# Kernel tuning notes

Measured on AMD Instinct MI355X. Metric: run time of the kernel, lower is better.

Reference implementation:

```python
import jax, jax.numpy as jnp
import numpy as np

H = 64       # hidden size hard-coded in the module
NH = 4       # n_heads
S = 500      # stock_num
D = 10       # num_day
T = 40       # num_text (news per day)
FP = 3       # price features
FT = 512     # text embedding dim


def gru_scan(x, Wih, Whh, bih, bhh):
    """Single-sequence GRU (torch gate convention). x: (T, F) -> hidden states (T, H)."""
    gi = x @ Wih + bih  # (T, 3H) precompute input gates outside the scan

    def step(h, g):
        gh = h @ Whh + bhh
        r = jax.nn.sigmoid(g[:H] + gh[:H])
        z = jax.nn.sigmoid(g[H:2 * H] + gh[H:2 * H])
        n = jnp.tanh(g[2 * H:] + r * gh[2 * H:])
        h_new = (1.0 - z) * n + z * h
        return h_new, h_new

    h0 = jnp.zeros((H,), x.dtype)
    _, hs = jax.lax.scan(step, h0, gi)
    return hs


def attn_pool(hs, W, v):
    """Additive attention pooling over time. hs: (T, H) -> (H,)."""
    scores = jnp.tanh(hs @ W) @ v          # (T,)
    alpha = jax.nn.softmax(scores)
    return alpha @ hs


def _gru_params(key, fin, scale=0.08):
    k1, k2, k3, k4 = jax.random.split(key, 4)
    return (jax.random.normal(k1, (S, fin, 3 * H)) * scale,
            jax.random.normal(k2, (S, H, 3 * H)) * scale,
            jax.random.normal(k3, (S, 3 * H)) * scale,
            jax.random.normal(k4, (S, 3 * H)) * scale)


def _attn_params(key, scale=0.08):
    k1, k2 = jax.random.split(key)
    return (jax.random.normal(k1, (S, H, H)) * scale,
            jax.random.normal(k2, (S, H)) * scale)


def setup_inputs() -> dict:
    key = jax.random.key(0)
    ks = jax.random.split(key, 20)
    inp = {}
    inp['text_input'] = jax.random.normal(ks[0], (S, D, T, FT), dtype=jnp.float32)
    inp['price_input'] = jax.random.normal(ks[1], (S, D, FP), dtype=jnp.float32)
    inp['label'] = jax.random.randint(ks[2], (S,), 0, 2)
    inp['adj'] = jnp.ones((S, S), dtype=jnp.float32)
    inp['train'] = 0
    # per-stock stacked parameters
    (inp['Wih_p'], inp['Whh_p'], inp['bih_p'], inp['bhh_p']) = _gru_params(ks[3], FP)
    (inp['Wa_p'], inp['va_p']) = _attn_params(ks[4])
    (inp['Wih_t'], inp['Whh_t'], inp['bih_t'], inp['bhh_t']) = _gru_params(ks[5], FT)
    (inp['Wa_t'], inp['va_t']) = _attn_params(ks[6])
    (inp['Wih_s'], inp['Whh_s'], inp['bih_s'], inp['bhh_s']) = _gru_params(ks[7], H)
    (inp['Wa_s'], inp['va_s']) = _attn_params(ks[8])
    inp['Wb'] = jax.random.normal(ks[9], (S, H, H, H)) * 0.05   # Bilinear weight (out,in1,in2)
    inp['bb'] = jax.random.normal(ks[10], (S, H)) * 0.05
    inp['Wbl'] = jax.random.normal(ks[11], (S, H, 2)) * 0.08
    inp['bbl'] = jax.random.normal(ks[12], (S, 2)) * 0.08
    # shared cross-stock self-attention projections and final fc
    inp['Wq'] = jax.random.normal(ks[13], (H, H)) * 0.08
    inp['bq'] = jax.random.normal(ks[14], (H,)) * 0.08
    inp['Wk'] = jax.random.normal(ks[15], (H, H)) * 0.08
    inp['bk'] = jax.random.normal(ks[16], (H,)) * 0.08
    inp['Wf'] = jax.random.normal(ks[17], (H, 2)) * 0.08
    inp['bf'] = jax.random.normal(ks[18], (2,)) * 0.08
    return inp


def _forward(text_input, price_input, label,
             Wih_p, Whh_p, bih_p, bhh_p, Wa_p, va_p,
             Wih_t, Whh_t, bih_t, bhh_t, Wa_t, va_t,
             Wih_s, Whh_s, bih_s, bhh_s, Wa_s, va_s,
             Wb, bb, Wbl, bbl, Wq, bq, Wk, bk, Wf, bf):
    # ---- per-stock price encoder: GRU over days + attention pooling ----
    def enc_price(x, a, b, c, d, W, v):
        return attn_pool(gru_scan(x, a, b, c, d), W, v)
    x_price = jax.vmap(enc_price)(price_input, Wih_p, Whh_p, bih_p, bhh_p, Wa_p, va_p)  # (S, H)

    # ---- per-stock, per-day text encoder ----
    def enc_text_stock(xdays, a, b, c, d, W, v):
        return jax.vmap(lambda x: attn_pool(gru_scan(x, a, b, c, d), W, v))(xdays)  # (D, H)
    news = jax.vmap(enc_text_stock)(text_input, Wih_t, Whh_t, bih_t, bhh_t, Wa_t, va_t)  # (S, D, H)

    # ---- per-stock sequence encoder over days ----
    text_vec = jax.vmap(enc_price)(news, Wih_s, Whh_s, bih_s, bhh_s, Wa_s, va_s)  # (S, H)

    # ---- bilinear fusion: tanh(Bilinear(text, price)) ----
    combined = jnp.tanh(jnp.einsum('si,skij,sj->sk', text_vec, Wb, x_price) + bb)  # (S, H)

    # ---- per-stock blending head ----
    out_1 = jnp.tanh(jnp.einsum('si,sik->sk', combined, Wbl) + bbl)  # (S, 2)

    # ---- cross-stock multi-head self-attention (q,k projected, v identity) ----
    dh = H // NH
    q = (combined @ Wq + bq).reshape(S, NH, dh)
    k = (combined @ Wk + bk).reshape(S, NH, dh)
    v = combined.reshape(S, NH, dh)
    scores = jnp.einsum('shd,thd->hst', q, k) / (dh ** 0.5)
    attn = jax.nn.softmax(scores, axis=-1)
    attn_out = jnp.einsum('hst,thd->shd', attn, v).reshape(S, H)

    x = jax.nn.elu(attn_out @ Wf + bf)  # (S, 2)
    output = jax.nn.softmax(x + out_1, axis=1)
    # faithful to the original: CrossEntropyLoss applied to already-softmaxed output
    logp = jax.nn.log_softmax(output, axis=1)
    loss = -jnp.mean(logp[jnp.arange(S), label])
    return loss, output


def reference(text_input, price_input, label, adj, train,
              Wih_p, Whh_p, bih_p, bhh_p, Wa_p, va_p,
              Wih_t, Whh_t, bih_t, bhh_t, Wa_t, va_t,
              Wih_s, Whh_s, bih_s, bhh_s, Wa_s, va_s,
              Wb, bb, Wbl, bbl, Wq, bq, Wk, bk, Wf, bf):
    return _forward(text_input, price_input, label,
                    Wih_p, Whh_p, bih_p, bhh_p, Wa_p, va_p,
                    Wih_t, Whh_t, bih_t, bhh_t, Wa_t, va_t,
                    Wih_s, Whh_s, bih_s, bhh_s, Wa_s, va_s,
                    Wb, bb, Wbl, bbl, Wq, bq, Wk, bk, Wf, bf)
```

## Files before the change

kernel.cpp:

```cpp
#include <hip/hip_runtime.h>

#define Sn 500
#define Dn 10
#define Tn 40
#define FPn 3
#define FTn 512
#define Hn 64
#define G3 192
#define NHn 4

typedef __attribute__((ext_vector_type(8))) short bf8_t;
typedef __attribute__((ext_vector_type(4))) float f4_t;

__device__ __forceinline__ unsigned short f2bf(float f) {
    union { float f; unsigned int u; } v; v.f = f;
    unsigned int r = v.u + 0x7fffu + ((v.u >> 16) & 1u);
    return (unsigned short)(r >> 16);
}
__device__ __forceinline__ float bflo(unsigned int u) {
    union { unsigned int u; float f; } v; v.u = u << 16; return v.f;
}
__device__ __forceinline__ float bfhi(unsigned int u) {
    union { unsigned int u; float f; } v; v.u = u & 0xffff0000u; return v.f;
}
__device__ __forceinline__ unsigned int cvtpk(float lo, float hi) {
    unsigned int r;
    asm("v_cvt_pk_bf16_f32 %0, %1, %2" : "=v"(r) : "v"(lo), "v"(hi));
    return r;
}
__device__ __forceinline__ float sigmoidf_(float x) { return 1.f / (1.f + __expf(-x)); }
__device__ __forceinline__ float tanhf_(float x) {
    x = fminf(15.f, fmaxf(-15.f, x));
    float e = __expf(2.f * x);
    return (e - 1.f) / (e + 1.f);
}
__device__ __forceinline__ float dot8(uint4 wv, f4_t hA, f4_t hB) {
    return bflo(wv.x) * hA[0] + bfhi(wv.x) * hA[1]
         + bflo(wv.y) * hA[2] + bfhi(wv.y) * hA[3]
         + bflo(wv.z) * hB[0] + bfhi(wv.z) * hB[1]
         + bflo(wv.w) * hB[2] + bfhi(wv.w) * hB[3];
}
union bfu { bf8_t v; unsigned int u[4]; };

__global__ __launch_bounds__(64, 1) void price_gru(
    const float* __restrict__ price, const float* __restrict__ Wih_p,
    const float* __restrict__ Whh_p, const float* __restrict__ bih_p,
    const float* __restrict__ bhh_p, const float* __restrict__ Wa_p,
    const float* __restrict__ va_p, float* __restrict__ xprice)
{
    __shared__ __align__(16) unsigned char smp[33160];
    unsigned char* whh2 = smp;
    unsigned char* wa2 = smp + 24576;
    float* hbuf = (float*)(smp + 32768);
    float* priceL = (float*)(smp + 33040);

    const int s = blockIdx.x, l = threadIdx.x;
    {
        const float* W3 = Whh_p + (size_t)s * Hn * G3;
        for (int r = 0; r < 192; ++r) {
            int e = l + r * 64, i = e / G3, j = e - i * G3;
            *(unsigned short*)(whh2 + j * 128 + ((2 * i) ^ ((j & 7) << 4))) = f2bf(W3[e]);
        }
        const float* A3 = Wa_p + (size_t)s * Hn * Hn;
        for (int r = 0; r < 64; ++r) {
            int e = l + r * 64, i = e >> 6, k = e & 63;
            *(unsigned short*)(wa2 + k * 128 + ((2 * i) ^ ((k & 7) << 4))) = f2bf(A3[e]);
        }
        if (l < 30) priceL[l] = price[(size_t)s * 30 + l];
        hbuf[l] = 0.f;
        if (l < 4) hbuf[64 + l] = 0.f;
    }
    __builtin_amdgcn_wave_barrier();
    {
        float wp[3][3];
        #pragma unroll
        for (int i = 0; i < 3; ++i)
            #pragma unroll
            for (int g = 0; g < 3; ++g)
                wp[i][g] = Wih_p[(size_t)s * 3 * G3 + i * G3 + g * 64 + l];
        const float bi0 = bih_p[(size_t)s * G3 + l];
        const float bi1 = bih_p[(size_t)s * G3 + 64 + l];
        const float bi2 = bih_p[(size_t)s * G3 + 128 + l];
        const float bh0 = bhh_p[(size_t)s * G3 + l];
        const float bh1 = bhh_p[(size_t)s * G3 + 64 + l];
        const float bh2 = bhh_p[(size_t)s * G3 + 128 + l];
        const float vak = va_p[(size_t)s * Hn + l];
        const int swl = (l & 7) << 4;
        float h3 = 0.f, m3 = -1e30f, den3 = 0.f, av3 = 0.f;
        for (int t = 0; t < Dn; ++t) {
            float x0 = priceL[t * 3], x1 = priceL[t * 3 + 1], x2 = priceL[t * 3 + 2];
            float gg0 = bi0 + x0 * wp[0][0] + x1 * wp[1][0] + x2 * wp[2][0];
            float gg1 = bi1 + x0 * wp[0][1] + x1 * wp[1][1] + x2 * wp[2][1];
            float gg2 = bi2 + x0 * wp[0][2] + x1 * wp[1][2] + x2 * wp[2][2];
            float gh0 = bh0, gh1 = bh1, gh2 = bh2;
            #pragma unroll
            for (int ic = 0; ic < 8; ++ic) {
                const int off = (ic * 16) ^ swl;
                f4_t hA = *(const f4_t*)&hbuf[ic * 8];
                f4_t hB = *(const f4_t*)&hbuf[ic * 8 + 4];
                uint4 w0 = *(const uint4*)(whh2 + l * 128 + off);
                uint4 w1 = *(const uint4*)(whh2 + (l + 64) * 128 + off);
                uint4 w2 = *(const uint4*)(whh2 + (l + 128) * 128 + off);
                gh0 += dot8(w0, hA, hB); gh1 += dot8(w1, hA, hB); gh2 += dot8(w2, hA, hB);
            }
            float r = sigmoidf_(gg0 + gh0);
            float z = sigmoidf_(gg1 + gh1);
            float n = tanhf_(gg2 + r * gh2);
            h3 = (1.f - z) * n + z * h3;
            __builtin_amdgcn_wave_barrier();
            hbuf[l] = h3;
            __builtin_amdgcn_wave_barrier();
            float sk = 0.f;
            #pragma unroll
            for (int ic = 0; ic < 8; ++ic) {
                const int off = (ic * 16) ^ swl;
                uint4 wv = *(const uint4*)(wa2 + l * 128 + off);
                f4_t hA = *(const f4_t*)&hbuf[ic * 8];
                f4_t hB = *(const f4_t*)&hbuf[ic * 8 + 4];
                sk += dot8(wv, hA, hB);
            }
            float term = tanhf_(sk) * vak;
            #pragma unroll
            for (int off = 32; off; off >>= 1) term += __shfl_xor(term, off);
            float mn = fmaxf(m3, term);
            float s0 = __expf(m3 - mn);
            float p = __expf(term - mn);
            den3 = den3 * s0 + p;
            av3 = av3 * s0 + p * h3;
            m3 = mn;
        }
        xprice[(size_t)s * Hn + l] = av3 / den3;
    }
}

__global__ __launch_bounds__(256) void k1_mega(
    const float* __restrict__ text, const float* __restrict__ Wih,
    const float* __restrict__ bih, float* __restrict__ gi2,
    const float* __restrict__ Wb, const float* __restrict__ xprice,
    float* __restrict__ u)
{
    __shared__ __align__(16) unsigned char sm[18688];

    const int bid = blockIdx.x, tid = threadIdx.x;
    const int xcd = bid & 7, ix = bid >> 3;
    const int swz = (xcd < 4 ? xcd * 563 : 2252 + (xcd - 4) * 562) + ix;
    const int grp = swz / 9, sub = swz - grp * 9;
    const int w = tid >> 6, l = tid & 63;

    if (sub < 5) {
        const int s = grp, fi = sub;
        const int lr = l & 15, kg = l >> 4;
        unsigned short* Asb = (unsigned short*)sm;
        unsigned char*  Bsb = sm + 6400;

        const float* xbase = text + ((size_t)s * 400 + fi * 80) * FTn;
        const float* Wihs  = Wih + (size_t)s * FTn * G3;

        f4_t acc[5][3];
        #pragma unroll
        for (int a = 0; a < 5; a++)
            #pragma unroll
            for (int b = 0; b < 3; b++) acc[a][b] = (f4_t){0.f, 0.f, 0.f, 0.f};

        f4_t pa[3];
        f4_t pb0[3], pb1[3];

        auto aload = [&](int kk) {
            #pragma unroll
            for (int q = 0; q < 3; ++q) {
                int t = tid + q * 256;
                if (q < 2 || tid < 128) {
                    int row = t >> 3, ch = t & 7;
                    pa[q] = *(const f4_t*)(xbase + (size_t)row * FTn + kk * 32 + ch * 4);
                }
            }
        };
        auto bload = [&](int kk) {
            #pragma unroll
            for (int q = 0; q < 3; ++q) {
                int t = tid + q * 256;
                int kp = t / 48, cq = t % 48;
                const float* p = Wihs + (size_t)(kk * 32 + 2 * kp) * G3 + cq * 4;
                pb0[q] = *(const f4_t*)p;
                pb1[q] = *(const f4_t*)(p + G3);
            }
        };
        auto awrite = [&]() {
            #pragma unroll
            for (int q = 0; q < 3; ++q) {
                int t = tid + q * 256;
                if (q < 2 || tid < 128) {
                    int row = t >> 3, ch = t & 7;
                    uint2 uu = { cvtpk(pa[q][0], pa[q][1]), cvtpk(pa[q][2], pa[q][3]) };
                    *(uint2*)((unsigned char*)Asb + row * 80 + ch * 8) = uu;
                }
            }
        };
        auto bwrite = [&]() {
            #pragma unroll
            for (int q = 0; q < 3; ++q) {
                int t = tid + q * 256;
                int kp = t / 48, cq = t % 48;
                int base = (kp >> 2) * 3072 + (kp & 3) * 4;
                #pragma unroll
                for (int i = 0; i < 4; ++i) {
                    int col = cq * 4 + i;
                    int colp = col ^ ((col >> 2) & 7);
                    *(unsigned int*)(Bsb + base + colp * 16) = cvtpk(pb0[q][i], pb1[q][i]);
                }
            }
        };

        aload(0); bload(0);
        for (int kk = 0; kk < 16; ++kk) {
            awrite(); bwrite();
            __syncthreads();
            if (kk < 15) { aload(kk + 1); bload(kk + 1); }
            bf8_t bfr[3];
            #pragma unroll
            for (int nc = 0; nc < 3; ++nc) {
                int col = w * 48 + nc * 16 + lr;
                int colp = col ^ ((col >> 2) & 7);
                bfr[nc] = *(const bf8_t*)(Bsb + kg * 3072 + colp * 16);
            }
            #pragma unroll
            for (int mt = 0; mt < 5; ++mt) {
                bf8_t af = *(const bf8_t*)((unsigned char*)Asb + (mt * 16 + lr) * 80 + kg * 16);
                acc[mt][0] = __builtin_amdgcn_mfma_f32_16x16x32_bf16(af, bfr[0], acc[mt][0], 0, 0, 0);
                acc[mt][1] = __builtin_amdgcn_mfma_f32_16x16x32_bf16(af, bfr[1], acc[mt][1], 0, 0, 0);
                acc[mt][2] = __builtin_amdgcn_mfma_f32_16x16x32_bf16(af, bfr[2], acc[mt][2], 0, 0, 0);
            }
            __syncthreads();
        }

        const float* bihs = bih + (size_t)s * G3 + w * 48 + lr;
        #pragma unroll
        for (int nc = 0; nc < 3; ++nc) {
            const int col = w * 48 + nc * 16 + lr;
            const float bv = bihs[nc * 16];
            #pragma unroll
            for (int mt = 0; mt < 5; ++mt)
                #pragma unroll
                for (int rg = 0; rg < 4; ++rg) {
                    int r = mt * 16 + kg * 4 + rg;
                    int hi = (r >= 40);
                    int day = fi * 2 + hi;
                    int t = r - hi * 40;
                    gi2[((size_t)(s * 40 + t) * 10 + day) * 192 + col] = acc[mt][nc][rg] + bv;
                }
        }
    } else {
        const int s = grp, kq = sub - 5;
        float* uT = (float*)sm;
        const int j4 = (l & 15) * 4;
        f4_t xq = *(const f4_t*)&xprice[s * Hn + j4];

        const float* Wbs = Wb + (size_t)s * Hn * Hn * Hn;
        for (int g = 0; g < 64; ++g) {
            int P = kq * 1024 + w * 256 + g * 4 + (l >> 4);
            f4_t wv = *(const f4_t*)&Wbs[(size_t)P * Hn + j4];
            float dp = wv[0] * xq[0] + wv[1] * xq[1] + wv[2] * xq[2] + wv[3] * xq[3];
            dp += __shfl_xor(dp, 8);
            dp += __shfl_xor(dp, 4);
            dp += __shfl_xor(dp, 2);
            dp += __shfl_xor(dp, 1);
            if ((l & 15) == 0) { int k = P >> 6, i = P & 63; uT[i * 17 + (k - kq * 16)] = dp; }
        }
        __syncthreads();
        #pragma unroll
        for (int r = 0; r < 4; ++r) {
            int flat = tid + r * 256;
            int kr = flat >> 6, i = flat & 63;
            u[((size_t)s * 64 + kq * 16 + kr) * 64 + i] = uT[i * 17 + kr];
        }
    }
}

__global__ __launch_bounds__(64, 1) void gru_text_f(
    const float* __restrict__ gi2, const float* __restrict__ Whh,
    const float* __restrict__ bhh, const float* __restrict__ Wa,
    const float* __restrict__ va, float* __restrict__ news)
{
    __shared__ __align__(16) float hrow[16 * 68];
    __shared__ __align__(16) unsigned char waT[Hn * 128];

    const int s = blockIdx.x, l = threadIdx.x;
    const int lr = l & 15, lg = l >> 4;

    const float* Whhs = Whh + (size_t)s * Hn * G3;
    bfu bwhh[2][12];
    #pragma unroll
    for (int ks = 0; ks < 2; ++ks)
        #pragma unroll
        for (int nt = 0; nt < 12; ++nt) {
            const float* p = Whhs + (size_t)(ks * 32 + lg * 8) * G3 + nt * 16 + lr;
            float b0 = p[0], b1 = p[G3], b2 = p[2 * G3], b3 = p[3 * G3];
            float b4 = p[4 * G3], b5 = p[5 * G3], b6 = p[6 * G3], b7 = p[7 * G3];
            bwhh[ks][nt].u[0] = cvtpk(b0, b1); bwhh[ks][nt].u[1] = cvtpk(b2, b3);
            bwhh[ks][nt].u[2] = cvtpk(b4, b5); bwhh[ks][nt].u[3] = cvtpk(b6, b7);
        }
    float bhh_l[12];
    #pragma unroll
    for (int nt = 0; nt < 12; ++nt) bhh_l[nt] = bhh[(size_t)s * G3 + nt * 16 + lr];
    float va_l[4];
    #pragma unroll
    for (int nt = 0; nt < 4; ++nt) va_l[nt] = va[(size_t)s * Hn + nt * 16 + lr];

    {
        const float* Was = Wa + (size_t)s * Hn * Hn;
        for (int r = 0; r < 64; ++r) {
            int e = l + r * 64, i = e >> 6, k = e & 63;
            *(unsigned short*)(waT + k * 128 + ((2 * i) ^ ((k & 7) << 4))) = f2bf(Was[e]);
        }
        #pragma unroll
        for (int r = 0; r < 17; ++r) hrow[l + r * 64] = 0.f;
    }
    __builtin_amdgcn_wave_barrier();

    int dayoff[4];
    #pragma unroll
    for (int rr = 0; rr < 4; ++rr) {
        int d = lg * 4 + rr; if (d > 9) d = 9;
        dayoff[rr] = d * 192 + lr;
    }
    const float* gbase = gi2 + (size_t)s * 40 * 1920;

    float val[48], valn[48];
    #pragma unroll
    for (int j = 0; j < 48; ++j) val[j] = gbase[dayoff[j & 3] + (j >> 2) * 16];

    bf8_t a0f, a1f;
    {   bfu z0; z0.u[0] = 0; z0.u[1] = 0; z0.u[2] = 0; z0.u[3] = 0; a0f = z0.v; a1f = z0.v; }

    float h[4][4], accv[4][4], den[4], m[4];
    #pragma unroll
    for (int nt = 0; nt < 4; ++nt)
        #pragma unroll
        for (int rr = 0; rr < 4; ++rr) { h[nt][rr] = 0.f; accv[nt][rr] = 0.f; }
    #pragma unroll
    for (int rr = 0; rr < 4; ++rr) { den[rr] = 0.f; m[rr] = -1e30f; }

    for (int t = 0; t < Tn; ++t) {
        f4_t acc[12];
        #pragma unroll
        for (int nt = 0; nt < 12; ++nt)
            acc[nt] = (f4_t){bhh_l[nt], bhh_l[nt], bhh_l[nt], bhh_l[nt]};
        __builtin_amdgcn_s_setprio(1);
        #pragma unroll
        for (int nt = 0; nt < 12; ++nt) {
            acc[nt] = __builtin_amdgcn_mfma_f32_16x16x32_bf16(a0f, bwhh[0][nt].v, acc[nt], 0, 0, 0);
            acc[nt] = __builtin_amdgcn_mfma_f32_16x16x32_bf16(a1f, bwhh[1][nt].v, acc[nt], 0, 0, 0);
        }
        __builtin_amdgcn_s_setprio(0);
        {
            const int tn = (t < Tn - 1) ? t + 1 : t;
            const float* gb = gbase + (size_t)tn * 1920;
            #pragma unroll
            for (int j = 0; j < 48; ++j) valn[j] = gb[dayoff[j & 3] + (j >> 2) * 16];
        }
        #pragma unroll
        for (int nt = 0; nt < 4; ++nt)
            #pragma unroll
            for (int rr = 0; rr < 4; ++rr) {
                float r = sigmoidf_(val[nt * 4 + rr] + acc[nt][rr]);
                float z = sigmoidf_(val[(nt + 4) * 4 + rr] + acc[nt + 4][rr]);
                float n = tanhf_(val[(nt + 8) * 4 + rr] + r * acc[nt + 8][rr]);
                h[nt][rr] = (1.f - z) * n + z * h[nt][rr];
            }
        __builtin_amdgcn_wave_barrier();
        #pragma unroll
        for (int rr = 0; rr < 4; ++rr) {
            int day = lg * 4 + rr;
            if (day < Dn) {
                #pragma unroll
                for (int nt = 0; nt < 4; ++nt) hrow[day * 68 + nt * 16 + lr] = h[nt][rr];
            }
        }
        __builtin_amdgcn_wave_barrier();
        {
            const float* hp = hrow + lr * 68 + lg * 8;
            f4_t x0 = *(const f4_t*)hp,        x1 = *(const f4_t*)(hp + 4);
            f4_t y0 = *(const f4_t*)(hp + 32), y1 = *(const f4_t*)(hp + 36);
            bfu t0, t1;
            t0.u[0] = cvtpk(x0[0], x0[1]); t0.u[1] = cvtpk(x0[2], x0[3]);
            t0.u[2] = cvtpk(x1[0], x1[1]); t0.u[3] = cvtpk(x1[2], x1[3]);
            t1.u[0] = cvtpk(y0[0], y0[1]); t1.u[1] = cvtpk(y0[2], y0[3]);
            t1.u[2] = cvtpk(y1[0], y1[1]); t1.u[3] = cvtpk(y1[2], y1[3]);
            a0f = t0.v; a1f = t1.v;
        }
        f4_t sc[4];
        #pragma unroll
        for (int nt = 0; nt < 4; ++nt) sc[nt] = (f4_t){0.f, 0.f, 0.f, 0.f};
        __builtin_amdgcn_s_setprio(1);
        #pragma unroll
        for (int ks = 0; ks < 2; ++ks) {
            bf8_t av = ks ? a1f : a0f;
            #pragma unroll
            for (int nt = 0; nt < 4; ++nt) {
                bf8_t bwv = *(const bf8_t*)(waT + (nt * 16 + lr) * 128
                                            + ((ks * 64 + lg * 16) ^ ((lr & 7) << 4)));
                sc[nt] = __builtin_amdgcn_mfma_f32_16x16x32_bf16(av, bwv, sc[nt], 0, 0, 0);
            }
        }
        __builtin_amdgcn_s_setprio(0);
        float pr[4];
        #pragma unroll
        for (int rr = 0; rr < 4; ++rr) {
            pr[rr] = tanhf_(sc[0][rr]) * va_l[0] + tanhf_(sc[1][rr]) * va_l[1]
                   + tanhf_(sc[2][rr]) * va_l[2] + tanhf_(sc[3][rr]) * va_l[3];
            pr[rr] += __shfl_xor(pr[rr], 1);
            pr[rr] += __shfl_xor(pr[rr], 2);
            pr[rr] += __shfl_xor(pr[rr], 4);
            pr[rr] += __shfl_xor(pr[rr], 8);
        }
        #pragma unroll
        for (int rr = 0; rr < 4; ++rr) {
            float mn = fmaxf(m[rr], pr[rr]);
            float s0 = __expf(m[rr] - mn);
            float p = __expf(pr[rr] - mn);
            den[rr] = den[rr] * s0 + p;
            #pragma unroll
            for (int nt = 0; nt < 4; ++nt)
                accv[nt][rr] = accv[nt][rr] * s0 + p * h[nt][rr];
            m[rr] = mn;
        }
        #pragma unroll
        for (int j = 0; j < 48; ++j) val[j] = valn[j];
    }
    #pragma unroll
    for (int rr = 0; rr < 4; ++rr) {
        int day = lg * 4 + rr;
        if (day < Dn) {
            float inv = 1.f / den[rr];
            #pragma unroll
            for (int nt = 0; nt < 4; ++nt)
                news[((size_t)s * Dn + day) * Hn + nt * 16 + lr] = accv[nt][rr] * inv;
        }
    }
}

__global__ __launch_bounds__(64, 1) void day_finish(
    const float* __restrict__ news,
    const float* __restrict__ Wih_s, const float* __restrict__ Whh_s,
    const float* __restrict__ bih_s, const float* __restrict__ bhh_s,
    const float* __restrict__ Wa_s, const float* __restrict__ va_s,
    const float* __restrict__ u, const float* __restrict__ bb,
    const float* __restrict__ Wq, const float* __restrict__ bq,
    const float* __restrict__ Wk, const float* __restrict__ bk,
    const float* __restrict__ Wbl, const float* __restrict__ bbl,
    float* __restrict__ combined, float* __restrict__ qg,
    float* __restrict__ kg, float* __restrict__ out1)
{
    __shared__ __align__(16) unsigned char sm[60928];
    unsigned char* whh2 = sm;
    unsigned char* wih2 = sm + 24576;
    unsigned char* wa2 = sm + 49152;
    float* newsL = (float*)(sm + 57600);
    float* hbuf  = (float*)(sm + 60320);

    const int s = blockIdx.x, l = threadIdx.x;
    float tvv;

    {
        const float* W2 = Whh_s + (size_t)s * Hn * G3;
        const float* X2 = Wih_s + (size_t)s * Hn * G3;
        for (int r = 0; r < 192; ++r) {
            int e = l + r * 64, i = e / G3, j = e - i * G3;
            int off = j * 128 + ((2 * i) ^ ((j & 7) << 4));
            *(unsigned short*)(whh2 + off) = f2bf(W2[e]);
            *(unsigned short*)(wih2 + off) = f2bf(X2[e]);
        }
        const float* A2 = Wa_s + (size_t)s * Hn * Hn;
        for (int r = 0; r < 64; ++r) {
            int e = l + r * 64, i = e >> 6, k = e & 63;
            *(unsigned short*)(wa2 + k * 128 + ((2 * i) ^ ((k & 7) << 4))) = f2bf(A2[e]);
        }
        #pragma unroll
        for (int d = 0; d < Dn; ++d) newsL[d * 68 + l] = news[((size_t)s * Dn + d) * Hn + l];
        hbuf[l] = 0.f;
        if (l < 4) hbuf[64 + l] = 0.f;
    }
    __builtin_amdgcn_wave_barrier();
    {
        const float bi0 = bih_s[(size_t)s * G3 + l];
        const float bi1 = bih_s[(size_t)s * G3 + 64 + l];
        const float bi2 = bih_s[(size_t)s * G3 + 128 + l];
        const float bh0 = bhh_s[(size_t)s * G3 + l];
        const float bh1 = bhh_s[(size_t)s * G3 + 64 + l];
        const float bh2 = bhh_s[(size_t)s * G3 + 128 + l];
        const float vak = va_s[(size_t)s * Hn + l];
        const int swl = (l & 7) << 4;
        float h2 = 0.f, m2 = -1e30f, den2 = 0.f, av2 = 0.f;
        for (int t = 0; t < Dn; ++t) {
            float gh0 = bh0, gh1 = bh1, gh2 = bh2;
            float gg0 = bi0, gg1 = bi1, gg2 = bi2;
            #pragma unroll
            for (int ic = 0; ic < 8; ++ic) {
                const int off = (ic * 16) ^ swl;
                f4_t hA = *(const f4_t*)&hbuf[ic * 8];
                f4_t hB = *(const f4_t*)&hbuf[ic * 8 + 4];
                f4_t nA = *(const f4_t*)&newsL[t * 68 + ic * 8];
                f4_t nB = *(const f4_t*)&newsL[t * 68 + ic * 8 + 4];
                uint4 w0 = *(const uint4*)(whh2 + l * 128 + off);
                uint4 w1 = *(const uint4*)(whh2 + (l + 64) * 128 + off);
                uint4 w2 = *(const uint4*)(whh2 + (l + 128) * 128 + off);
                uint4 x0 = *(const uint4*)(wih2 + l * 128 + off);
                uint4 x1 = *(const uint4*)(wih2 + (l + 64) * 128 + off);
                uint4 x2 = *(const uint4*)(wih2 + (l + 128) * 128 + off);
                gh0 += dot8(w0, hA, hB); gh1 += dot8(w1, hA, hB); gh2 += dot8(w2, hA, hB);
                gg0 += dot8(x0, nA, nB); gg1 += dot8(x1, nA, nB); gg2 += dot8(x2, nA, nB);
            }
            float r = sigmoidf_(gg0 + gh0);
            float z = sigmoidf_(gg1 + gh1);
            float n = tanhf_(gg2 + r * gh2);
            h2 = (1.f - z) * n + z * h2;
            __builtin_amdgcn_wave_barrier();
            hbuf[l] = h2;
            __builtin_amdgcn_wave_barrier();
            float sk = 0.f;
            #pragma unroll
            for (int ic = 0; ic < 8; ++ic) {
                const int off = (ic * 16) ^ swl;
                uint4 wv = *(const uint4*)(wa2 + l * 128 + off);
                f4_t hA = *(const f4_t*)&hbuf[ic * 8];
                f4_t hB = *(const f4_t*)&hbuf[ic * 8 + 4];
                sk += dot8(wv, hA, hB);
            }
            float term = tanhf_(sk) * vak;
            #pragma unroll
            for (int off = 32; off; off >>= 1) term += __shfl_xor(term, off);
            float mn = fmaxf(m2, term);
            float s0 = __expf(m2 - mn);
            float p = __expf(term - mn);
            den2 = den2 * s0 + p;
            av2 = av2 * s0 + p * h2;
            m2 = mn;
        }
        tvv = av2 / den2;
    }
    __builtin_amdgcn_wave_barrier();

    float* uL = (float*)sm;
    float* tvL = (float*)(sm + 16640);
    float* cl  = (float*)(sm + 16960);
    tvL[l] = tvv;
    const float* ub = u + (size_t)s * 4096;
    #pragma unroll 8
    for (int i = 0; i < 64; ++i) uL[i * 65 + l] = ub[i * 64 + l];
    __builtin_amdgcn_wave_barrier();
    {
        float a = bb[s * Hn + l];
        #pragma unroll 8
        for (int i = 0; i < 64; ++i) a += tvL[i] * uL[l * 65 + i];
        float c = tanhf_(a);
        cl[l] = c;
        combined[s * Hn + l] = c;
    }
    __builtin_amdgcn_wave_barrier();
    {
        float aq = bq[l], ak = bk[l];
        for (int i = 0; i < Hn; i++) {
            float ci = cl[i];
            aq += ci * Wq[i * Hn + l];
            ak += ci * Wk[i * Hn + l];
        }
        qg[s * Hn + l] = aq; kg[s * Hn + l] = ak;
        if (l < 2) {
            float a = bbl[s * 2 + l];
            for (int i = 0; i < Hn; i++) a += cl[i] * Wbl[(size_t)s * Hn * 2 + i * 2 + l];
            out1[s * 2 + l] = tanhf_(a);
        }
    }
}

__global__ __launch_bounds__(256) void mhsa(
    const float* __restrict__ qg, const float* __restrict__ kg,
    const float* __restrict__ combined, const float* __restrict__ Wf,
    const float* __restrict__ bfp, const float* __restrict__ out1,
    float* __restrict__ dout)
{
    __shared__ __align__(16) float ql[Hn];
    __shared__ float sl[NHn][Sn];
    __shared__ float hsum[NHn];
    __shared__ float ao[Hn];
    __shared__ float red2[8];
    __shared__ float red3[4][Hn];

    const int sq = blockIdx.x, tid = threadIdx.x;
    if (tid < Hn) ql[tid] = qg[sq * Hn + tid];
    __syncthreads();

    for (int id = tid; id < Sn * NHn; id += 256) {
        int t = id >> 2, h = id & 3;
        const float* kp = &kg[t * Hn + h * 16];
        float a = 0.f;
        #pragma unroll
        for (int x = 0; x < 16; x += 4) {
            f4_t kv = *(const f4_t*)&kp[x];
            f4_t qv = *(const f4_t*)&ql[h * 16 + x];
            a += kv[0] * qv[0] + kv[1] * qv[1] + kv[2] * qv[2] + kv[3] * qv[3];
        }
        sl[h][t] = a * 0.25f;
    }
    __syncthreads();
    for (int h = 0; h < NHn; ++h) {
        float m = -1e30f;
        for (int t = tid; t < Sn; t += 256) m = fmaxf(m, sl[h][t]);
        for (int o = 32; o; o >>= 1) m = fmaxf(m, __shfl_xor(m, o));
        if ((tid & 63) == 0) red2[tid >> 6] = m;
        __syncthreads();
        m = fmaxf(fmaxf(red2[0], red2[1]), fmaxf(red2[2], red2[3]));
        float ps = 0.f;
        for (int t = tid; t < Sn; t += 256) { float p = __expf(sl[h][t] - m); sl[h][t] = p; ps += p; }
        for (int o = 32; o; o >>= 1) ps += __shfl_xor(ps, o);
        if ((tid & 63) == 0) red2[4 + (tid >> 6)] = ps;
        __syncthreads();
        if (tid == 0) hsum[h] = red2[4] + red2[5] + red2[6] + red2[7];
        __syncthreads();
    }
    {
        const int q = tid >> 6, j = tid & 63, h = j >> 4;
        float a = 0.f;
        for (int t = q * 125; t < q * 125 + 125; ++t) a += sl[h][t] * combined[t * Hn + j];
        red3[q][j] = a;
    }
    __syncthreads();
    if (tid < Hn)
        ao[tid] = (red3[0][tid] + red3[1][tid] + red3[2][tid] + red3[3][tid]) / hsum[tid >> 4];
    __syncthreads();
    if (tid == 0) {
        float l0 = bfp[0], l1 = bfp[1];
        for (int j = 0; j < Hn; j++) { float v = ao[j]; l0 += v * Wf[j * 2]; l1 += v * Wf[j * 2 + 1]; }
        l0 = l0 > 0.f ? l0 : __expf(l0) - 1.f;
        l1 = l1 > 0.f ? l1 : __expf(l1) - 1.f;
        l0 += out1[sq * 2]; l1 += out1[sq * 2 + 1];
        float m = fmaxf(l0, l1);
        float e0 = __expf(l0 - m), e1 = __expf(l1 - m);
        float inv = 1.f / (e0 + e1);
        dout[1 + sq * 2] = e0 * inv;
        dout[2 + sq * 2] = e1 * inv;
    }
}

__global__ __launch_bounds__(512) void loss_k(float* __restrict__ dout,
                                              const int* __restrict__ label)
{
    __shared__ float red[512];
    const int tid = threadIdx.x;
    float a = 0.f;
    if (tid < Sn) {
        float p0 = dout[1 + 2 * tid], p1 = dout[2 + 2 * tid];
        float m = fmaxf(p0, p1);
        float lse = m + __logf(__expf(p0 - m) + __expf(p1 - m));
        float pl = label[tid] ? p1 : p0;
        a = -(pl - lse);
    }
    red[tid] = a;
    __syncthreads();
    for (int o = 256; o; o >>= 1) {
        if (tid < o) red[tid] += red[tid + o];
        __syncthreads();
    }
    if (tid == 0) dout[0] = red[0] / (float)Sn;
}

extern "C" void kernel_launch(void* const* d_in, const int* in_sizes, int n_in,
                              void* d_out, int out_size, void* d_ws, size_t ws_size,
                              hipStream_t stream)
{
    const float* text  = (const float*)d_in[0];
    const float* price = (const float*)d_in[1];
    const int*   label = (const int*)  d_in[2];
    const float* Wih_p = (const float*)d_in[5];
    const float* Whh_p = (const float*)d_in[6];
    const float* bih_p = (const float*)d_in[7];
    const float* bhh_p = (const float*)d_in[8];
    const float* Wa_p  = (const float*)d_in[9];
    const float* va_p  = (const float*)d_in[10];
    const float* Wih_t = (const float*)d_in[11];
    const float* Whh_t = (const float*)d_in[12];
    const float* bih_t = (const float*)d_in[13];
    const float* bhh_t = (const float*)d_in[14];
    const float* Wa_t  = (const float*)d_in[15];
    const float* va_t  = (const float*)d_in[16];
    const float* Wih_s = (const float*)d_in[17];
    const float* Whh_s = (const float*)d_in[18];
    const float* bih_s = (const float*)d_in[19];
    const float* bhh_s = (const float*)d_in[20];
    const float* Wa_s  = (const float*)d_in[21];
    const float* va_s  = (const float*)d_in[22];
    const float* Wb    = (const float*)d_in[23];
    const float* bb    = (const float*)d_in[24];
    const float* Wbl   = (const float*)d_in[25];
    const float* bbl   = (const float*)d_in[26];
    const float* Wq    = (const float*)d_in[27];
    const float* bq    = (const float*)d_in[28];
    const float* Wk    = (const float*)d_in[29];
    const float* bk    = (const float*)d_in[30];
    const float* Wf    = (const float*)d_in[31];
    const float* bf_   = (const float*)d_in[32];

    float* ws = (float*)d_ws;
    float* news     = ws;
    float* xprice   = ws + 320000;
    float* combined = ws + 384000;
    float* qg       = ws + 416000;
    float* kg       = ws + 448000;
    float* out1     = ws + 480000;
    float* u        = ws + 481000;
    float* gi2      = ws + 2529000;
    float* dout = (float*)d_out;

    price_gru<<<Sn, 64, 0, stream>>>(price, Wih_p, Whh_p, bih_p, bhh_p, Wa_p, va_p, xprice);
    k1_mega<<<4500, 256, 0, stream>>>(text, Wih_t, bih_t, gi2, Wb, xprice, u);
    gru_text_f<<<Sn, 64, 0, stream>>>(gi2, Whh_t, bhh_t, Wa_t, va_t, news);
    day_finish<<<Sn, 64, 0, stream>>>(news,
                                      Wih_s, Whh_s, bih_s, bhh_s, Wa_s, va_s,
                                      u, bb, Wq, bq, Wk, bk, Wbl, bbl,
                                      combined, qg, kg, out1);
    mhsa<<<Sn, 256, 0, stream>>>(qg, kg, combined, Wf, bf_, out1, dout);
    loss_k<<<1, 512, 0, stream>>>(dout, label);
}
```

Measured before the change: 580.9 us.

## Double-buffer k1 LDS tiles and fuse text GRU with day-level kernel

The k1_mega GEMM now uses two LDS buffers. The next tile is converted and written while the current one feeds the MFMAs, which removes one barrier per k-step but doubles LDS per block and may lower occupancy. The text-GRU kernel is also merged into the day-level kernel. The per-day news vectors now stay in shared memory instead of going through global memory, and one launch is dropped.

```diff
diff --git a/kernel.cpp b/kernel.cpp
--- a/kernel.cpp
+++ b/kernel.cpp
@@ -139,7 +139,7 @@
     const float* __restrict__ Wb, const float* __restrict__ xprice,
     float* __restrict__ u)
 {
-    __shared__ __align__(16) unsigned char sm[18688];
+    __shared__ __align__(16) unsigned char sm[37376];
 
     const int bid = blockIdx.x, tid = threadIdx.x;
     const int xcd = bid & 7, ix = bid >> 3;
@@ -150,8 +150,8 @@
     if (sub < 5) {
         const int s = grp, fi = sub;
         const int lr = l & 15, kg = l >> 4;
-        unsigned short* Asb = (unsigned short*)sm;
-        unsigned char*  Bsb = sm + 6400;
+        unsigned char* Ab0 = sm;
+        unsigned char* Ab1 = sm + 18688;
 
         const float* xbase = text + ((size_t)s * 400 + fi * 80) * FTn;
         const float* Wihs  = Wih + (size_t)s * FTn * G3;
@@ -185,51 +185,55 @@
                 pb1[q] = *(const f4_t*)(p + G3);
             }
         };
-        auto awrite = [&]() {
+        auto awrite = [&](unsigned char* base) {
             #pragma unroll
             for (int q = 0; q < 3; ++q) {
                 int t = tid + q * 256;
                 if (q < 2 || tid < 128) {
                     int row = t >> 3, ch = t & 7;
                     uint2 uu = { cvtpk(pa[q][0], pa[q][1]), cvtpk(pa[q][2], pa[q][3]) };
-                    *(uint2*)((unsigned char*)Asb + row * 80 + ch * 8) = uu;
+                    *(uint2*)(base + row * 80 + ch * 8) = uu;
                 }
             }
         };
-        auto bwrite = [&]() {
+        auto bwrite = [&](unsigned char* base) {
             #pragma unroll
             for (int q = 0; q < 3; ++q) {
                 int t = tid + q * 256;
                 int kp = t / 48, cq = t % 48;
-                int base = (kp >> 2) * 3072 + (kp & 3) * 4;
+                int off = (kp >> 2) * 3072 + (kp & 3) * 4;
                 #pragma unroll
                 for (int i = 0; i < 4; ++i) {
                     int col = cq * 4 + i;
                     int colp = col ^ ((col >> 2) & 7);
-                    *(unsigned int*)(Bsb + base + colp * 16) = cvtpk(pb0[q][i], pb1[q][i]);
+                    *(unsigned int*)(base + 6400 + off + colp * 16) = cvtpk(pb0[q][i], pb1[q][i]);
                 }
             }
         };
 
         aload(0); bload(0);
+        awrite(Ab0); bwrite(Ab0);
+        __syncthreads();
+
         for (int kk = 0; kk < 16; ++kk) {
-            awrite(); bwrite();
-            __syncthreads();
+            unsigned char* cur = (kk & 1) ? Ab1 : Ab0;
+            unsigned char* nxt = (kk & 1) ? Ab0 : Ab1;
             if (kk < 15) { aload(kk + 1); bload(kk + 1); }
             bf8_t bfr[3];
             #pragma unroll
             for (int nc = 0; nc < 3; ++nc) {
                 int col = w * 48 + nc * 16 + lr;
                 int colp = col ^ ((col >> 2) & 7);
-                bfr[nc] = *(const bf8_t*)(Bsb + kg * 3072 + colp * 16);
+                bfr[nc] = *(const bf8_t*)(cur + 6400 + kg * 3072 + colp * 16);
             }
             #pragma unroll
             for (int mt = 0; mt < 5; ++mt) {
-                bf8_t af = *(const bf8_t*)((unsigned char*)Asb + (mt * 16 + lr) * 80 + kg * 16);
+                bf8_t af = *(const bf8_t*)(cur + (mt * 16 + lr) * 80 + kg * 16);
                 acc[mt][0] = __builtin_amdgcn_mfma_f32_16x16x32_bf16(af, bfr[0], acc[mt][0], 0, 0, 0);
                 acc[mt][1] = __builtin_amdgcn_mfma_f32_16x16x32_bf16(af, bfr[1], acc[mt][1], 0, 0, 0);
                 acc[mt][2] = __builtin_amdgcn_mfma_f32_16x16x32_bf16(af, bfr[2], acc[mt][2], 0, 0, 0);
             }
+            if (kk < 15) { awrite(nxt); bwrite(nxt); }
             __syncthreads();
         }
 
@@ -276,171 +280,10 @@
     }
 }
 
-__global__ __launch_bounds__(64, 1) void gru_text_f(
+__global__ __launch_bounds__(64, 1) void text_day(
     const float* __restrict__ gi2, const float* __restrict__ Whh,
     const float* __restrict__ bhh, const float* __restrict__ Wa,
-    const float* __restrict__ va, float* __restrict__ news)
-{
-    __shared__ __align__(16) float hrow[16 * 68];
-    __shared__ __align__(16) unsigned char waT[Hn * 128];
-
-    const int s = blockIdx.x, l = threadIdx.x;
-    const int lr = l & 15, lg = l >> 4;
-
-    const float* Whhs = Whh + (size_t)s * Hn * G3;
-    bfu bwhh[2][12];
-    #pragma unroll
-    for (int ks = 0; ks < 2; ++ks)
-        #pragma unroll
-        for (int nt = 0; nt < 12; ++nt) {
-            const float* p = Whhs + (size_t)(ks * 32 + lg * 8) * G3 + nt * 16 + lr;
-            float b0 = p[0], b1 = p[G3], b2 = p[2 * G3], b3 = p[3 * G3];
-            float b4 = p[4 * G3], b5 = p[5 * G3], b6 = p[6 * G3], b7 = p[7 * G3];
-            bwhh[ks][nt].u[0] = cvtpk(b0, b1); bwhh[ks][nt].u[1] = cvtpk(b2, b3);
-            bwhh[ks][nt].u[2] = cvtpk(b4, b5); bwhh[ks][nt].u[3] = cvtpk(b6, b7);
-        }
-    float bhh_l[12];
-    #pragma unroll
-    for (int nt = 0; nt < 12; ++nt) bhh_l[nt] = bhh[(size_t)s * G3 + nt * 16 + lr];
-    float va_l[4];
-    #pragma unroll
-    for (int nt = 0; nt < 4; ++nt) va_l[nt] = va[(size_t)s * Hn + nt * 16 + lr];
-
-    {
-        const float* Was = Wa + (size_t)s * Hn * Hn;
-        for (int r = 0; r < 64; ++r) {
-            int e = l + r * 64, i = e >> 6, k = e & 63;
-            *(unsigned short*)(waT + k * 128 + ((2 * i) ^ ((k & 7) << 4))) = f2bf(Was[e]);
-        }
-        #pragma unroll
-        for (int r = 0; r < 17; ++r) hrow[l + r * 64] = 0.f;
-    }
-    __builtin_amdgcn_wave_barrier();
-
-    int dayoff[4];
-    #pragma unroll
-    for (int rr = 0; rr < 4; ++rr) {
-        int d = lg * 4 + rr; if (d > 9) d = 9;
-        dayoff[rr] = d * 192 + lr;
-    }
-    const float* gbase = gi2 + (size_t)s * 40 * 1920;
-
-    float val[48], valn[48];
-    #pragma unroll
-    for (int j = 0; j < 48; ++j) val[j] = gbase[dayoff[j & 3] + (j >> 2) * 16];
-
-    bf8_t a0f, a1f;
-    {   bfu z0; z0.u[0] = 0; z0.u[1] = 0; z0.u[2] = 0; z0.u[3] = 0; a0f = z0.v; a1f = z0.v; }
-
-    float h[4][4], accv[4][4], den[4], m[4];
-    #pragma unroll
-    for (int nt = 0; nt < 4; ++nt)
-        #pragma unroll
-        for (int rr = 0; rr < 4; ++rr) { h[nt][rr] = 0.f; accv[nt][rr] = 0.f; }
-    #pragma unroll
-    for (int rr = 0; rr < 4; ++rr) { den[rr] = 0.f; m[rr] = -1e30f; }
-
-    for (int t = 0; t < Tn; ++t) {
-        f4_t acc[12];
-        #pragma unroll
-        for (int nt = 0; nt < 12; ++nt)
-            acc[nt] = (f4_t){bhh_l[nt], bhh_l[nt], bhh_l[nt], bhh_l[nt]};
-        __builtin_amdgcn_s_setprio(1);
-        #pragma unroll
-        for (int nt = 0; nt < 12; ++nt) {
-            acc[nt] = __builtin_amdgcn_mfma_f32_16x16x32_bf16(a0f, bwhh[0][nt].v, acc[nt], 0, 0, 0);
-            acc[nt] = __builtin_amdgcn_mfma_f32_16x16x32_bf16(a1f, bwhh[1][nt].v, acc[nt], 0, 0, 0);
-        }
-        __builtin_amdgcn_s_setprio(0);
-        {
-            const int tn = (t < Tn - 1) ? t + 1 : t;
-            const float* gb = gbase + (size_t)tn * 1920;
-            #pragma unroll
-            for (int j = 0; j < 48; ++j) valn[j] = gb[dayoff[j & 3] + (j >> 2) * 16];
-        }
-        #pragma unroll
-        for (int nt = 0; nt < 4; ++nt)
-            #pragma unroll
-            for (int rr = 0; rr < 4; ++rr) {
-                float r = sigmoidf_(val[nt * 4 + rr] + acc[nt][rr]);
-                float z = sigmoidf_(val[(nt + 4) * 4 + rr] + acc[nt + 4][rr]);
-                float n = tanhf_(val[(nt + 8) * 4 + rr] + r * acc[nt + 8][rr]);
-                h[nt][rr] = (1.f - z) * n + z * h[nt][rr];
-            }
-        __builtin_amdgcn_wave_barrier();
-        #pragma unroll
-        for (int rr = 0; rr < 4; ++rr) {
-            int day = lg * 4 + rr;
-            if (day < Dn) {
-                #pragma unroll
-                for (int nt = 0; nt < 4; ++nt) hrow[day * 68 + nt * 16 + lr] = h[nt][rr];
-            }
-        }
-        __builtin_amdgcn_wave_barrier();
-        {
-            const float* hp = hrow + lr * 68 + lg * 8;
-            f4_t x0 = *(const f4_t*)hp,        x1 = *(const f4_t*)(hp + 4);
-            f4_t y0 = *(const f4_t*)(hp + 32), y1 = *(const f4_t*)(hp + 36);
-            bfu t0, t1;
-            t0.u[0] = cvtpk(x0[0], x0[1]); t0.u[1] = cvtpk(x0[2], x0[3]);
-            t0.u[2] = cvtpk(x1[0], x1[1]); t0.u[3] = cvtpk(x1[2], x1[3]);
-            t1.u[0] = cvtpk(y0[0], y0[1]); t1.u[1] = cvtpk(y0[2], y0[3]);
-            t1.u[2] = cvtpk(y1[0], y1[1]); t1.u[3] = cvtpk(y1[2], y1[3]);
-            a0f = t0.v; a1f = t1.v;
-        }
-        f4_t sc[4];
-        #pragma unroll
-        for (int nt = 0; nt < 4; ++nt) sc[nt] = (f4_t){0.f, 0.f, 0.f, 0.f};
-        __builtin_amdgcn_s_setprio(1);
-        #pragma unroll
-        for (int ks = 0; ks < 2; ++ks) {
-            bf8_t av = ks ? a1f : a0f;
-            #pragma unroll
-            for (int nt = 0; nt < 4; ++nt) {
-                bf8_t bwv = *(const bf8_t*)(waT + (nt * 16 + lr) * 128
-                                            + ((ks * 64 + lg * 16) ^ ((lr & 7) << 4)));
-                sc[nt] = __builtin_amdgcn_mfma_f32_16x16x32_bf16(av, bwv, sc[nt], 0, 0, 0);
-            }
-        }
-        __builtin_amdgcn_s_setprio(0);
-        float pr[4];
-        #pragma unroll
-        for (int rr = 0; rr < 4; ++rr) {
-            pr[rr] = tanhf_(sc[0][rr]) * va_l[0] + tanhf_(sc[1][rr]) * va_l[1]
-                   + tanhf_(sc[2][rr]) * va_l[2] + tanhf_(sc[3][rr]) * va_l[3];
-            pr[rr] += __shfl_xor(pr[rr], 1);
-            pr[rr] += __shfl_xor(pr[rr], 2);
-            pr[rr] += __shfl_xor(pr[rr], 4);
-            pr[rr] += __shfl_xor(pr[rr], 8);
-        }
-        #pragma unroll
-        for (int rr = 0; rr < 4; ++rr) {
-            float mn = fmaxf(m[rr], pr[rr]);
-            float s0 = __expf(m[rr] - mn);
-            float p = __expf(pr[rr] - mn);
-            den[rr] = den[rr] * s0 + p;
-            #pragma unroll
-            for (int nt = 0; nt < 4; ++nt)
-                accv[nt][rr] = accv[nt][rr] * s0 + p * h[nt][rr];
-            m[rr] = mn;
-        }
-        #pragma unroll
-        for (int j = 0; j < 48; ++j) val[j] = valn[j];
-    }
-    #pragma unroll
-    for (int rr = 0; rr < 4; ++rr) {
-        int day = lg * 4 + rr;
-        if (day < Dn) {
-            float inv = 1.f / den[rr];
-            #pragma unroll
-            for (int nt = 0; nt < 4; ++nt)
-                news[((size_t)s * Dn + day) * Hn + nt * 16 + lr] = accv[nt][rr] * inv;
-        }
-    }
-}
-
-__global__ __launch_bounds__(64, 1) void day_finish(
-    const float* __restrict__ news,
+    const float* __restrict__ va,
     const float* __restrict__ Wih_s, const float* __restrict__ Whh_s,
     const float* __restrict__ bih_s, const float* __restrict__ bhh_s,
     const float* __restrict__ Wa_s, const float* __restrict__ va_s,
@@ -452,15 +295,173 @@
     float* __restrict__ kg, float* __restrict__ out1)
 {
     __shared__ __align__(16) unsigned char sm[60928];
+    float* hrow = (float*)sm;
+    unsigned char* waT = sm + 4352;
+    float* newsL = (float*)(sm + 57600);
     unsigned char* whh2 = sm;
     unsigned char* wih2 = sm + 24576;
-    unsigned char* wa2 = sm + 49152;
-    float* newsL = (float*)(sm + 57600);
-    float* hbuf  = (float*)(sm + 60320);
+    unsigned char* wa2  = sm + 49152;
+    float* hbuf = (float*)(sm + 60320);
 
     const int s = blockIdx.x, l = threadIdx.x;
+    const int lr = l & 15, lg = l >> 4;
+
+    {
+        const float* Whhs = Whh + (size_t)s * Hn * G3;
+        bfu bwhh[2][12];
+        #pragma unroll
+        for (int ks = 0; ks < 2; ++ks)
+            #pragma unroll
+            for (int nt = 0; nt < 12; ++nt) {
+                const float* p = Whhs + (size_t)(ks * 32 + lg * 8) * G3 + nt * 16 + lr;
+                float b0 = p[0], b1 = p[G3], b2 = p[2 * G3], b3 = p[3 * G3];
+                float b4 = p[4 * G3], b5 = p[5 * G3], b6 = p[6 * G3], b7 = p[7 * G3];
+                bwhh[ks][nt].u[0] = cvtpk(b0, b1); bwhh[ks][nt].u[1] = cvtpk(b2, b3);
+                bwhh[ks][nt].u[2] = cvtpk(b4, b5); bwhh[ks][nt].u[3] = cvtpk(b6, b7);
+            }
+        float bhh_l[12];
+        #pragma unroll
+        for (int nt = 0; nt < 12; ++nt) bhh_l[nt] = bhh[(size_t)s * G3 + nt * 16 + lr];
+        float va_l[4];
+        #pragma unroll
+        for (int nt = 0; nt < 4; ++nt) va_l[nt] = va[(size_t)s * Hn + nt * 16 + lr];
+
+        {
+            const float* Was = Wa + (size_t)s * Hn * Hn;
+            for (int r = 0; r < 64; ++r) {
+                int e = l + r * 64, i = e >> 6, k = e & 63;
+                *(unsigned short*)(waT + k * 128 + ((2 * i) ^ ((k & 7) << 4))) = f2bf(Was[e]);
+            }
+            #pragma unroll
+            for (int r = 0; r < 17; ++r) hrow[l + r * 64] = 0.f;
+        }
+        __builtin_amdgcn_wave_barrier();
+
+        int dayoff[4];
+        #pragma unroll
+        for (int rr = 0; rr < 4; ++rr) {
+            int d = lg * 4 + rr; if (d > 9) d = 9;
+            dayoff[rr] = d * 192 + lr;
+        }
+        const float* gbase = gi2 + (size_t)s * 40 * 1920;
+
+        float val[48], valn[48];
+        #pragma unroll
+        for (int j = 0; j < 48; ++j) val[j] = gbase[dayoff[j & 3] + (j >> 2) * 16];
+
+        bf8_t a0f, a1f;
+        {   bfu z0; z0.u[0] = 0; z0.u[1] = 0; z0.u[2] = 0; z0.u[3] = 0; a0f = z0.v; a1f = z0.v; }
+
+        float h[4][4], accv[4][4], den[4], m[4];
+        #pragma unroll
+        for (int nt = 0; nt < 4; ++nt)
+            #pragma unroll
+            for (int rr = 0; rr < 4; ++rr) { h[nt][rr] = 0.f; accv[nt][rr] = 0.f; }
+        #pragma unroll
+        for (int rr = 0; rr < 4; ++rr) { den[rr] = 0.f; m[rr] = -1e30f; }
+
+        for (int t = 0; t < Tn; ++t) {
+            f4_t acc[12];
+            #pragma unroll
+            for (int nt = 0; nt < 12; ++nt)
+                acc[nt] = (f4_t){bhh_l[nt], bhh_l[nt], bhh_l[nt], bhh_l[nt]};
+            __builtin_amdgcn_s_setprio(1);
+            #pragma unroll
+            for (int nt = 0; nt < 12; ++nt) {
+                acc[nt] = __builtin_amdgcn_mfma_f32_16x16x32_bf16(a0f, bwhh[0][nt].v, acc[nt], 0, 0, 0);
+                acc[nt] = __builtin_amdgcn_mfma_f32_16x16x32_bf16(a1f, bwhh[1][nt].v, acc[nt], 0, 0, 0);
+            }
+            __builtin_amdgcn_s_setprio(0);
+            {
+                const int tn = (t < Tn - 1) ? t + 1 : t;
+                const float* gb = gbase + (size_t)tn * 1920;
+                #pragma unroll
+                for (int j = 0; j < 48; ++j) valn[j] = gb[dayoff[j & 3] + (j >> 2) * 16];
+            }
+            #pragma unroll
+            for (int nt = 0; nt < 4; ++nt)
+                #pragma unroll
+                for (int rr = 0; rr < 4; ++rr) {
+                    float r = sigmoidf_(val[nt * 4 + rr] + acc[nt][rr]);
+                    float z = sigmoidf_(val[(nt + 4) * 4 + rr] + acc[nt + 4][rr]);
+                    float n = tanhf_(val[(nt + 8) * 4 + rr] + r * acc[nt + 8][rr]);
+                    h[nt][rr] = (1.f - z) * n + z * h[nt][rr];
+                }
+            __builtin_amdgcn_wave_barrier();
+            #pragma unroll
+            for (int rr = 0; rr < 4; ++rr) {
+                int day = lg * 4 + rr;
+                if (day < Dn) {
+                    #pragma unroll
+                    for (int nt = 0; nt < 4; ++nt) hrow[day * 68 + nt * 16 + lr] = h[nt][rr];
+                }
+            }
+            __builtin_amdgcn_wave_barrier();
+            {
+                const float* hp = hrow + lr * 68 + lg * 8;
+                f4_t x0 = *(const f4_t*)hp,        x1 = *(const f4_t*)(hp + 4);
+                f4_t y0 = *(const f4_t*)(hp + 32), y1 = *(const f4_t*)(hp + 36);
+                bfu t0, t1;
+                t0.u[0] = cvtpk(x0[0], x0[1]); t0.u[1] = cvtpk(x0[2], x0[3]);
+                t0.u[2] = cvtpk(x1[0], x1[1]); t0.u[3] = cvtpk(x1[2], x1[3]);
+                t1.u[0] = cvtpk(y0[0], y0[1]); t1.u[1] = cvtpk(y0[2], y0[3]);
+                t1.u[2] = cvtpk(y1[0], y1[1]); t1.u[3] = cvtpk(y1[2], y1[3]);
+                a0f = t0.v; a1f = t1.v;
+            }
+            f4_t sc[4];
+            #pragma unroll
+            for (int nt = 0; nt < 4; ++nt) sc[nt] = (f4_t){0.f, 0.f, 0.f, 0.f};
+            __builtin_amdgcn_s_setprio(1);
+            #pragma unroll
+            for (int ks = 0; ks < 2; ++ks) {
+                bf8_t av = ks ? a1f : a0f;
+                #pragma unroll
+                for (int nt = 0; nt < 4; ++nt) {
+                    bf8_t bwv = *(const bf8_t*)(waT + (nt * 16 + lr) * 128
+                                                + ((ks * 64 + lg * 16) ^ ((lr & 7) << 4)));
+                    sc[nt] = __builtin_amdgcn_mfma_f32_16x16x32_bf16(av, bwv, sc[nt], 0, 0, 0);
+                }
+            }
+            __builtin_amdgcn_s_setprio(0);
+            float pr[4];
+            #pragma unroll
+            for (int rr = 0; rr < 4; ++rr) {
+                pr[rr] = tanhf_(sc[0][rr]) * va_l[0] + tanhf_(sc[1][rr]) * va_l[1]
+                       + tanhf_(sc[2][rr]) * va_l[2] + tanhf_(sc[3][rr]) * va_l[3];
+                pr[rr] += __shfl_xor(pr[rr], 1);
+                pr[rr] += __shfl_xor(pr[rr], 2);
+                pr[rr] += __shfl_xor(pr[rr], 4);
+                pr[rr] += __shfl_xor(pr[rr], 8);
+            }
+            #pragma unroll
+            for (int rr = 0; rr < 4; ++rr) {
+                float mn = fmaxf(m[rr], pr[rr]);
+                float s0 = __expf(m[rr] - mn);
+                float p = __expf(pr[rr] - mn);
+                den[rr] = den[rr] * s0 + p;
+                #pragma unroll
+                for (int nt = 0; nt < 4; ++nt)
+                    accv[nt][rr] = accv[nt][rr] * s0 + p * h[nt][rr];
+                m[rr] = mn;
+            }
+            #pragma unroll
+            for (int j = 0; j < 48; ++j) val[j] = valn[j];
+        }
+        __builtin_amdgcn_wave_barrier();
+        #pragma unroll
+        for (int rr = 0; rr < 4; ++rr) {
+            int day = lg * 4 + rr;
+            if (day < Dn) {
+                float inv = 1.f / den[rr];
+                #pragma unroll
+                for (int nt = 0; nt < 4; ++nt)
+                    newsL[day * 68 + nt * 16 + lr] = accv[nt][rr] * inv;
+            }
+        }
+        __builtin_amdgcn_wave_barrier();
+    }
+
     float tvv;
-
     {
         const float* W2 = Whh_s + (size_t)s * Hn * G3;
         const float* X2 = Wih_s + (size_t)s * Hn * G3;
@@ -475,8 +476,6 @@
             int e = l + r * 64, i = e >> 6, k = e & 63;
             *(unsigned short*)(wa2 + k * 128 + ((2 * i) ^ ((k & 7) << 4))) = f2bf(A2[e]);
         }
-        #pragma unroll
-        for (int d = 0; d < Dn; ++d) newsL[d * 68 + l] = news[((size_t)s * Dn + d) * Hn + l];
         hbuf[l] = 0.f;
         if (l < 4) hbuf[64 + l] = 0.f;
     }
@@ -701,7 +700,6 @@
     const float* bf_   = (const float*)d_in[32];
 
     float* ws = (float*)d_ws;
-    float* news     = ws;
     float* xprice   = ws + 320000;
     float* combined = ws + 384000;
     float* qg       = ws + 416000;
@@ -713,11 +711,10 @@
 
     price_gru<<<Sn, 64, 0, stream>>>(price, Wih_p, Whh_p, bih_p, bhh_p, Wa_p, va_p, xprice);
     k1_mega<<<4500, 256, 0, stream>>>(text, Wih_t, bih_t, gi2, Wb, xprice, u);
-    gru_text_f<<<Sn, 64, 0, stream>>>(gi2, Whh_t, bhh_t, Wa_t, va_t, news);
-    day_finish<<<Sn, 64, 0, stream>>>(news,
-                                      Wih_s, Whh_s, bih_s, bhh_s, Wa_s, va_s,
-                                      u, bb, Wq, bq, Wk, bk, Wbl, bbl,
-                                      combined, qg, kg, out1);
+    text_day<<<Sn, 64, 0, stream>>>(gi2, Whh_t, bhh_t, Wa_t, va_t,
+                                    Wih_s, Whh_s, bih_s, bhh_s, Wa_s, va_s,
+                                    u, bb, Wq, bq, Wk, bk, Wbl, bbl,
+                                    combined, qg, kg, out1);
     mhsa<<<Sn, 256, 0, stream>>>(qg, kg, combined, Wf, bf_, out1, dout);
     loss_k<<<1, 512, 0, stream>>>(dout, label);
 }
```

Measured after the change: 597.4 us. 2.8% more time.
